# Optimization experiments

Measured on AMD Instinct MI355X. Metric: run time of the kernel, lower is better.

Reference implementation:

```python
import jax, jax.numpy as jnp
import numpy as np

N_NODES = 100000
N_EDGES = 600000
D = 128
HEADS = 8
REL = 9
N_GRAPHS = 64


def _relconv(h, coeff, basis, w_loop, b, src, dst, etypes, n_nodes):
    # DGL RelGraphConv, basis regularizer (num_bases == num_rels), sum aggregation,
    # self-loop, bias, relu activation (dropout inactive at eval).
    W = jnp.einsum('rb,bio->rio', coeff, basis)  # [REL, D, D]
    hsrc = h[src]                                # [E, D] gather
    msg = jnp.zeros((hsrc.shape[0], W.shape[2]), h.dtype)
    for r in range(REL):  # small fixed relation set
        msg = msg + jnp.where((etypes == r)[:, None], hsrc @ W[r], 0.0)
    agg = jax.ops.segment_sum(msg, dst, num_segments=n_nodes)
    return jax.nn.relu(agg + h @ w_loop + b)


def _graph_norm(x, seg, n_graphs, w, b, ms):
    # scatter-based per-subgraph normalization (graphNorm)
    counts = jax.ops.segment_sum(jnp.ones((x.shape[0],), x.dtype), seg, num_segments=n_graphs)[:, None]
    mean = jax.ops.segment_sum(x, seg, num_segments=n_graphs) / counts
    sub = x - mean[seg] * ms
    var = jax.ops.segment_sum(sub * sub, seg, num_segments=n_graphs) / counts
    std = jnp.sqrt(var + 1e-6)
    return w * sub / std[seg] + b


def _layer_norm(x, g, b):
    mu = x.mean(-1, keepdims=True)
    v = jnp.mean((x - mu) ** 2, -1, keepdims=True)
    return g * (x - mu) / jnp.sqrt(v + 1e-5) + b


def _forward(h, src, dst, etypes, seg, num_graphs,
             q_coeff, q_basis, q_loop, q_bias,
             k_coeff, k_basis, k_loop, k_bias,
             v_coeff, v_basis, v_loop, v_bias,
             o_w, o_b, gn1_w, gn1_b, gn1_ms, ln1_g, ln1_b,
             gn2_w, gn2_b, gn2_ms, ffn1_w, ffn1_b, ffn2_w, ffn2_b,
             ln2_g, ln2_b):
    n = h.shape[0]
    hn = _graph_norm(h, seg, num_graphs, gn1_w, gn1_b, gn1_ms)
    Q = _relconv(hn, q_coeff, q_basis, q_loop, q_bias, src, dst, etypes, n)
    K = _relconv(hn, k_coeff, k_basis, k_loop, k_bias, src, dst, etypes, n)
    V = _relconv(hn, v_coeff, v_basis, v_loop, v_bias, src, dst, etypes, n)
    dh = D // HEADS
    Qh = Q.reshape(n, HEADS, dh)
    Kh = K.reshape(n, HEADS, dh)
    Vh = V.reshape(n, HEADS, dh)
    # edge dot-product attention: score_e = <K[src], Q[dst]> per head
    score = (Kh[src] * Qh[dst]).sum(-1, keepdims=True)            # [E, H, 1]
    score = jnp.exp(jnp.clip(score / np.float32(np.sqrt(dh)), -10.0, 10.0))
    wV = jax.ops.segment_sum(Vh[src] * score, dst, num_segments=n)  # [N, H, dh]
    z = jax.ops.segment_sum(score, dst, num_segments=n)             # [N, H, 1]
    attn = (wV / (z + 1e-6)).reshape(n, D)
    hO = attn @ o_w + o_b
    h1 = _layer_norm(hO, ln1_g, ln1_b)
    h2 = _graph_norm(h1, seg, num_graphs, gn2_w, gn2_b, gn2_ms)
    h3 = jax.nn.relu(h2 @ ffn1_w + ffn1_b) @ ffn2_w + ffn2_b
    return _layer_norm(h3, ln2_g, ln2_b)


def setup_inputs() -> dict:
    key = jax.random.key(0)
    ks = jax.random.split(key, 32)
    s = np.float32(1.0 / np.sqrt(D))
    inp = {
        'h': jax.random.normal(ks[0], (N_NODES, D), jnp.float32),
        'src': jax.random.randint(ks[1], (N_EDGES,), 0, N_NODES),
        'dst': jax.random.randint(ks[2], (N_EDGES,), 0, N_NODES),
        'etypes': jax.random.randint(ks[3], (N_EDGES,), 0, REL),
        'seg': jnp.sort(jax.random.randint(ks[4], (N_NODES,), 0, N_GRAPHS)),
        'num_graphs': N_GRAPHS,
    }
    def lin(k, i, o):
        return jax.random.normal(k, (i, o), jnp.float32) / np.float32(np.sqrt(i))
    for idx, nm in enumerate(['q', 'k', 'v']):
        base = 5 + idx * 4
        inp[nm + '_coeff'] = jax.random.normal(ks[base], (REL, REL), jnp.float32) / np.float32(np.sqrt(REL))
        inp[nm + '_basis'] = jax.random.normal(ks[base + 1], (REL, D, D), jnp.float32) * s
        inp[nm + '_loop'] = lin(ks[base + 2], D, D)
        inp[nm + '_bias'] = jnp.zeros((D,), jnp.float32)
    inp['o_w'] = lin(ks[17], D, D)
    inp['o_b'] = jnp.zeros((D,), jnp.float32)
    for nm in ['gn1', 'gn2']:
        inp[nm + '_w'] = jnp.ones((D,), jnp.float32)
        inp[nm + '_b'] = jnp.zeros((D,), jnp.float32)
        inp[nm + '_ms'] = jnp.ones((D,), jnp.float32)
    inp['ln1_g'] = jnp.ones((D,), jnp.float32)
    inp['ln1_b'] = jnp.zeros((D,), jnp.float32)
    inp['ln2_g'] = jnp.ones((D,), jnp.float32)
    inp['ln2_b'] = jnp.zeros((D,), jnp.float32)
    inp['ffn1_w'] = lin(ks[18], D, 2 * D)
    inp['ffn1_b'] = jnp.zeros((2 * D,), jnp.float32)
    inp['ffn2_w'] = lin(ks[19], 2 * D, D)
    inp['ffn2_b'] = jnp.zeros((D,), jnp.float32)
    return inp


def reference(h, src, dst, etypes, seg, num_graphs,
              q_coeff, q_basis, q_loop, q_bias,
              k_coeff, k_basis, k_loop, k_bias,
              v_coeff, v_basis, v_loop, v_bias,
              o_w, o_b, gn1_w, gn1_b, gn1_ms, ln1_g, ln1_b,
              gn2_w, gn2_b, gn2_ms, ffn1_w, ffn1_b, ffn2_w, ffn2_b,
              ln2_g, ln2_b):
    return _forward(h, src, dst, etypes, seg, num_graphs,
                    q_coeff, q_basis, q_loop, q_bias,
                    k_coeff, k_basis, k_loop, k_bias,
                    v_coeff, v_basis, v_loop, v_bias,
                    o_w, o_b, gn1_w, gn1_b, gn1_ms, ln1_g, ln1_b,
                    gn2_w, gn2_b, gn2_ms, ffn1_w, ffn1_b, ffn2_w, ffn2_b,
                    ln2_g, ln2_b)
```

## Files before the change

kernel.cpp:

```cpp
#include <hip/hip_runtime.h>
#include <math.h>

#define N_NODES 100000
#define N_EDGES 600000
#define D 128
#define REL 9
#define NG 64

typedef float f32x4 __attribute__((ext_vector_type(4)));
typedef _Float16 f16x8 __attribute__((ext_vector_type(8)));

__device__ __forceinline__ ushort f2h(float x) {
    union { _Float16 h; ushort u; } c; c.h = (_Float16)x; return c.u;
}
__device__ __forceinline__ float h2f(ushort u) {
    union { ushort u; _Float16 h; } c; c.u = u; return (float)c.h;
}

__device__ __forceinline__ void ld16(const ushort* g, ushort* l) {
    __builtin_amdgcn_global_load_lds(
        (const __attribute__((address_space(1))) unsigned int*)g,
        (__attribute__((address_space(3))) unsigned int*)l, 16, 0, 0);
}

__device__ __forceinline__ int lbound(const int* __restrict__ a, int n, int key) {
    int lo = 0, hi = n;
    while (lo < hi) { int mid = (lo + hi) >> 1; if (a[mid] < key) lo = mid + 1; else hi = mid; }
    return lo;
}

__global__ void hist_kernel(const int* __restrict__ dst, int* __restrict__ cnt) {
    int e = blockIdx.x * 256 + threadIdx.x;
    if (e < N_EDGES) atomicAdd(&cnt[dst[e]], 1);
}

__global__ void scan1_kernel(const int* __restrict__ cnt, int* __restrict__ excl,
                             int* __restrict__ bsum, int n) {
    __shared__ int s[1024];
    int tid = threadIdx.x;
    int i = blockIdx.x * 1024 + tid;
    int v = (i < n) ? cnt[i] : 0;
    s[tid] = v;
    __syncthreads();
    for (int off = 1; off < 1024; off <<= 1) {
        int t = (tid >= off) ? s[tid - off] : 0;
        __syncthreads();
        s[tid] += t;
        __syncthreads();
    }
    if (i < n) excl[i] = s[tid] - v;
    if (tid == 1023) bsum[blockIdx.x] = s[1023];
}

__global__ void scan2_kernel(int* __restrict__ bsum, int nb) {
    __shared__ int s[128];
    int tid = threadIdx.x;
    int v = (tid < nb) ? bsum[tid] : 0;
    s[tid] = v;
    __syncthreads();
    for (int off = 1; off < 128; off <<= 1) {
        int t = (tid >= off) ? s[tid - off] : 0;
        __syncthreads();
        s[tid] += t;
        __syncthreads();
    }
    if (tid < nb) bsum[tid] = s[tid] - v;
}

__global__ void scan3_kernel(int* __restrict__ excl, const int* __restrict__ bsum, int n) {
    int i = blockIdx.x * 1024 + threadIdx.x;
    if (i < n) excl[i] += bsum[blockIdx.x];
}

__global__ void scatter_kernel(const int* __restrict__ src, const int* __restrict__ dst,
                               const int* __restrict__ ety, const int* __restrict__ estart,
                               int* __restrict__ cur, int* __restrict__ ssrc,
                               int* __restrict__ setp) {
    int e = blockIdx.x * 256 + threadIdx.x;
    if (e < N_EDGES) {
        int d = dst[e];
        int pos = estart[d] + atomicAdd(&cur[d], 1);
        ssrc[pos] = src[e];
        setp[pos] = ety[e];
    }
}

__global__ __launch_bounds__(256)
void gn_stats(const float* __restrict__ x, const int* __restrict__ seg,
              float* __restrict__ gsum, float* __restrict__ gsumsq) {
    int ch = threadIdx.x & 127;
    int rr = threadIdx.x >> 7;
    int n0 = blockIdx.x * 128;
    int nend = min(n0 + 128, N_NODES);
    float sx = 0.f, sxx = 0.f;
    int cg = -1;
    for (int n = n0 + rr; n < nend; n += 2) {
        int g = seg[n];
        if (g != cg) {
            if (cg >= 0) { atomicAdd(&gsum[cg * D + ch], sx); atomicAdd(&gsumsq[cg * D + ch], sxx); }
            cg = g; sx = 0.f; sxx = 0.f;
        }
        float v = x[(size_t)n * D + ch];
        sx += v; sxx += v * v;
    }
    if (cg >= 0) { atomicAdd(&gsum[cg * D + ch], sx); atomicAdd(&gsumsq[cg * D + ch], sxx); }
}

__global__ __launch_bounds__(256)
void gn_stats_h(const ushort* __restrict__ x, const int* __restrict__ seg,
                float* __restrict__ gsum, float* __restrict__ gsumsq) {
    int ch = threadIdx.x & 127;
    int rr = threadIdx.x >> 7;
    int n0 = blockIdx.x * 128;
    int nend = min(n0 + 128, N_NODES);
    float sx = 0.f, sxx = 0.f;
    int cg = -1;
    for (int n = n0 + rr; n < nend; n += 2) {
        int g = seg[n];
        if (g != cg) {
            if (cg >= 0) { atomicAdd(&gsum[cg * D + ch], sx); atomicAdd(&gsumsq[cg * D + ch], sxx); }
            cg = g; sx = 0.f; sxx = 0.f;
        }
        float v = h2f(x[(size_t)n * D + ch]);
        sx += v; sxx += v * v;
    }
    if (cg >= 0) { atomicAdd(&gsum[cg * D + ch], sx); atomicAdd(&gsumsq[cg * D + ch], sxx); }
}

__global__ void gn_final(const float* __restrict__ gsum, const float* __restrict__ gsumsq,
                         const int* __restrict__ seg, const float* __restrict__ w,
                         const float* __restrict__ b, const float* __restrict__ ms,
                         float* __restrict__ sc, float* __restrict__ off) {
    int g = blockIdx.x, ch = threadIdx.x;
    int lo = lbound(seg, N_NODES, g), hi = lbound(seg, N_NODES, g + 1);
    float cnt = (float)max(hi - lo, 1);
    float mean = gsum[g * D + ch] / cnt;
    float mm = mean * ms[ch];
    float var = gsumsq[g * D + ch] / cnt - 2.f * mm * mean + mm * mm;
    float rstd = rsqrtf(var + 1e-6f);
    float s = w[ch] * rstd;
    sc[g * D + ch] = s;
    off[g * D + ch] = b[ch] - s * mm;
}

__global__ __launch_bounds__(256)
void gn_apply(const float* __restrict__ x, const int* __restrict__ seg,
              const float* __restrict__ sc, const float* __restrict__ off,
              ushort* __restrict__ outhf) {
    int t = blockIdx.x * 256 + threadIdx.x;
    int n = t >> 6;
    if (n >= N_NODES) return;
    int ch = (t & 63) * 2;
    int g = seg[n];
    float2 xv = *(const float2*)&x[(size_t)n * D + ch];
    float2 s2 = *(const float2*)&sc[g * D + ch];
    float2 o2 = *(const float2*)&off[g * D + ch];
    ushort2 o;
    o.x = f2h(s2.x * xv.x + o2.x);
    o.y = f2h(s2.y * xv.y + o2.y);
    *(ushort2*)&outhf[(size_t)n * D + ch] = o;
}

__global__ __launch_bounds__(256)
void gn_apply_h(const ushort* __restrict__ x, const int* __restrict__ seg,
                const float* __restrict__ sc, const float* __restrict__ off,
                ushort* __restrict__ outhf) {
    int t = blockIdx.x * 256 + threadIdx.x;
    int n = t >> 6;
    if (n >= N_NODES) return;
    int ch = (t & 63) * 2;
    int g = seg[n];
    ushort2 xv = *(const ushort2*)&x[(size_t)n * D + ch];
    float2 s2 = *(const float2*)&sc[g * D + ch];
    float2 o2 = *(const float2*)&off[g * D + ch];
    ushort2 o;
    o.x = f2h(s2.x * h2f(xv.x) + o2.x);
    o.y = f2h(s2.y * h2f(xv.y) + o2.y);
    *(ushort2*)&outhf[(size_t)n * D + ch] = o;
}

__global__ void build_bt_qkv(const float* __restrict__ coeff, const float* __restrict__ basis,
                             const float* __restrict__ loop_w, const float* __restrict__ bias_in,
                             ushort* __restrict__ Bt, float* __restrict__ bias_out) {
    int t = blockIdx.x * 256 + threadIdx.x;
    if (t < 128) bias_out[t] = bias_in[t];
    if (t >= 128 * 1280) return;
    int o = t / 1280;
    int k = t - o * 1280;
    float v;
    if (k < 128) {
        v = loop_w[k * 128 + o];
    } else {
        int kk = k - 128;
        int r = kk >> 7, i = kk & 127;
        v = 0.f;
#pragma unroll
        for (int b = 0; b < REL; ++b)
            v += coeff[r * REL + b] * basis[((size_t)b * 128 + i) * 128 + o];
    }
    Bt[(size_t)o * 1280 + k] = f2h(v);
}

__global__ void transpose_cast(const float* __restrict__ W, int I, int O, ushort* __restrict__ Bt) {
    int t = blockIdx.x * 256 + threadIdx.x;
    if (t >= I * O) return;
    int n = t / I, k = t - n * I;
    Bt[(size_t)n * I + k] = f2h(W[(size_t)k * O + n]);
}

__global__ __launch_bounds__(256)
void s_pass(const ushort* __restrict__ hnhf, const int* __restrict__ ssrc,
            const int* __restrict__ setp, const int* __restrict__ estart,
            const int* __restrict__ ecnt, ushort* __restrict__ Ab, int c0, int c1) {
    int n = c0 + ((blockIdx.x * 256 + threadIdx.x) >> 6);
    if (n >= c1) return;
    int lane = threadIdx.x & 63;
    int e0 = estart[n], e1 = e0 + ecnt[n];
    float ax0=0,ay0=0,ax1=0,ay1=0,ax2=0,ay2=0,ax3=0,ay3=0,ax4=0,ay4=0;
    float ax5=0,ay5=0,ax6=0,ay6=0,ax7=0,ay7=0,ax8=0,ay8=0;
    for (int e = e0; e < e1; ++e) {
        int s = ssrc[e];
        int r = __builtin_amdgcn_readfirstlane(setp[e]);
        ushort2 hv = *(const ushort2*)&hnhf[(size_t)s * D + 2 * lane];
        float vx = h2f(hv.x), vy = h2f(hv.y);
        switch (r) {
            case 0: ax0 += vx; ay0 += vy; break;
            case 1: ax1 += vx; ay1 += vy; break;
            case 2: ax2 += vx; ay2 += vy; break;
            case 3: ax3 += vx; ay3 += vy; break;
            case 4: ax4 += vx; ay4 += vy; break;
            case 5: ax5 += vx; ay5 += vy; break;
            case 6: ax6 += vx; ay6 += vy; break;
            case 7: ax7 += vx; ay7 += vy; break;
            default: ax8 += vx; ay8 += vy; break;
        }
    }
    ushort* arow = Ab + (size_t)(n - c0) * 1152;
    ushort2 t;
#define ST(r) t.x = f2h(ax##r); t.y = f2h(ay##r); *(ushort2*)&arow[r * 128 + 2 * lane] = t;
    ST(0) ST(1) ST(2) ST(3) ST(4) ST(5) ST(6) ST(7) ST(8)
#undef ST
}

template<bool SPLITA, bool RELU, bool F16OUT>
__global__ __launch_bounds__(256, 3)
void mfma_gemm(const ushort* __restrict__ A1, const ushort* __restrict__ A2, int lda2, int M,
               const ushort* __restrict__ Bt, int K,
               const float* __restrict__ bias, void* __restrict__ Cout, int ldc) {
    __shared__ ushort As[128 * 64];
    __shared__ ushort Bs[128 * 64];
    const int tid = threadIdx.x;
    const int lane = tid & 63;
    const int wave = tid >> 6;
    const int wm = wave & 1, wn = wave >> 1;
    const int quad = lane >> 4, l16 = lane & 15;
    const int col0 = blockIdx.x * 128, row0 = blockIdx.y * 128;

    const ushort* sA1[4];
    const ushort* sA2[4];
    const ushort* sB[4];
#pragma unroll
    for (int i = 0; i < 4; ++i) {
        int rs = (wave * 4 + i) * 8 + (lane >> 3);
        int kg = (lane & 7) ^ (rs & 7);
        int ra = row0 + rs; if (ra >= M) ra = M - 1;
        sA1[i] = SPLITA ? (A1 + (size_t)ra * 128 + kg * 8) : nullptr;
        sA2[i] = A2 + (size_t)ra * lda2 + kg * 8;
        sB[i]  = Bt + (size_t)(col0 + rs) * K + kg * 8;
    }

    f32x4 acc[4][4];
#pragma unroll
    for (int i = 0; i < 4; ++i)
#pragma unroll
        for (int j = 0; j < 4; ++j) acc[i][j] = (f32x4){0.f, 0.f, 0.f, 0.f};

    for (int kc = 0; kc < K; kc += 64) {
#pragma unroll
        for (int i = 0; i < 4; ++i) {
            const ushort* as = (SPLITA && kc < 128) ? (sA1[i] + kc) : (sA2[i] + (SPLITA ? kc - 128 : kc));
            ld16(as, &As[(wave * 4 + i) * 512]);
            ld16(sB[i] + kc, &Bs[(wave * 4 + i) * 512]);
        }
        __syncthreads();
#pragma unroll
        for (int h = 0; h < 2; ++h) {
            f16x8 af[4], bf[4];
#pragma unroll
            for (int i = 0; i < 4; ++i) {
                int r = wm * 64 + i * 16 + l16;
                af[i] = *(const f16x8*)&As[r * 64 + (((h * 4 + quad) ^ (r & 7)) * 8)];
                int c = wn * 64 + i * 16 + l16;
                bf[i] = *(const f16x8*)&Bs[c * 64 + (((h * 4 + quad) ^ (c & 7)) * 8)];
            }
#pragma unroll
            for (int i = 0; i < 4; ++i)
#pragma unroll
                for (int j = 0; j < 4; ++j)
                    acc[i][j] = __builtin_amdgcn_mfma_f32_16x16x32_f16(af[i], bf[j], acc[i][j], 0, 0, 0);
        }
        __syncthreads();
    }

#pragma unroll
    for (int i = 0; i < 4; ++i) {
        int gr0 = row0 + wm * 64 + i * 16 + quad * 4;
#pragma unroll
        for (int r = 0; r < 4; ++r) {
            int grow = gr0 + r;
            if (grow >= M) continue;
#pragma unroll
            for (int j = 0; j < 4; ++j) {
                int gcol = col0 + wn * 64 + j * 16 + l16;
                float v = acc[i][j][r] + bias[gcol];
                if (RELU) v = fmaxf(v, 0.f);
                if (F16OUT) ((ushort*)Cout)[(size_t)grow * ldc + gcol] = f2h(v);
                else        ((float*)Cout)[(size_t)grow * ldc + gcol] = v;
            }
        }
    }
}

template<bool F16OUT>
__global__ __launch_bounds__(256, 3)
void mfma_gemm_ln(const ushort* __restrict__ A, int lda, int M,
                  const ushort* __restrict__ Bt, int K,
                  const float* __restrict__ bias, const float* __restrict__ lng,
                  const float* __restrict__ lnb, void* __restrict__ Cout) {
    __shared__ ushort As[128 * 64];
    __shared__ ushort Bs[128 * 64];
    __shared__ float rsum[2][128];
    __shared__ float rsq[2][128];
    const int tid = threadIdx.x;
    const int lane = tid & 63;
    const int wave = tid >> 6;
    const int wm = wave & 1, wn = wave >> 1;
    const int quad = lane >> 4, l16 = lane & 15;
    const int row0 = blockIdx.y * 128;

    const ushort* sA[4];
    const ushort* sB[4];
#pragma unroll
    for (int i = 0; i < 4; ++i) {
        int rs = (wave * 4 + i) * 8 + (lane >> 3);
        int kg = (lane & 7) ^ (rs & 7);
        int ra = row0 + rs; if (ra >= M) ra = M - 1;
        sA[i] = A + (size_t)ra * lda + kg * 8;
        sB[i] = Bt + (size_t)rs * K + kg * 8;
    }

    f32x4 acc[4][4];
#pragma unroll
    for (int i = 0; i < 4; ++i)
#pragma unroll
        for (int j = 0; j < 4; ++j) acc[i][j] = (f32x4){0.f, 0.f, 0.f, 0.f};

    for (int kc = 0; kc < K; kc += 64) {
#pragma unroll
        for (int i = 0; i < 4; ++i) {
            ld16(sA[i] + kc, &As[(wave * 4 + i) * 512]);
            ld16(sB[i] + kc, &Bs[(wave * 4 + i) * 512]);
        }
        __syncthreads();
#pragma unroll
        for (int h = 0; h < 2; ++h) {
            f16x8 af[4], bf[4];
#pragma unroll
            for (int i = 0; i < 4; ++i) {
                int r = wm * 64 + i * 16 + l16;
                af[i] = *(const f16x8*)&As[r * 64 + (((h * 4 + quad) ^ (r & 7)) * 8)];
                int c = wn * 64 + i * 16 + l16;
                bf[i] = *(const f16x8*)&Bs[c * 64 + (((h * 4 + quad) ^ (c & 7)) * 8)];
            }
#pragma unroll
            for (int i = 0; i < 4; ++i)
#pragma unroll
                for (int j = 0; j < 4; ++j)
                    acc[i][j] = __builtin_amdgcn_mfma_f32_16x16x32_f16(af[i], bf[j], acc[i][j], 0, 0, 0);
        }
        __syncthreads();
    }

#pragma unroll
    for (int i = 0; i < 4; ++i) {
#pragma unroll
        for (int r = 0; r < 4; ++r) {
            float s = 0.f, q = 0.f;
#pragma unroll
            for (int j = 0; j < 4; ++j) {
                float v = acc[i][j][r] + bias[wn * 64 + j * 16 + l16];
                s += v; q += v * v;
            }
            s += __shfl_xor(s, 1); q += __shfl_xor(q, 1);
            s += __shfl_xor(s, 2); q += __shfl_xor(q, 2);
            s += __shfl_xor(s, 4); q += __shfl_xor(q, 4);
            s += __shfl_xor(s, 8); q += __shfl_xor(q, 8);
            if (l16 == 0) {
                int row = wm * 64 + i * 16 + quad * 4 + r;
                rsum[wn][row] = s;
                rsq[wn][row] = q;
            }
        }
    }
    __syncthreads();

#pragma unroll
    for (int i = 0; i < 4; ++i) {
#pragma unroll
        for (int r = 0; r < 4; ++r) {
            int row = wm * 64 + i * 16 + quad * 4 + r;
            int grow = row0 + row;
            if (grow >= M) continue;
            float tot = rsum[0][row] + rsum[1][row];
            float tq  = rsq[0][row] + rsq[1][row];
            float mu = tot * (1.f / 128.f);
            float var = tq * (1.f / 128.f) - mu * mu;
            float rstd = rsqrtf(var + 1e-5f);
#pragma unroll
            for (int j = 0; j < 4; ++j) {
                int gcol = wn * 64 + j * 16 + l16;
                float v = acc[i][j][r] + bias[gcol];
                float o = lng[gcol] * (v - mu) * rstd + lnb[gcol];
                if (F16OUT) ((ushort*)Cout)[(size_t)grow * 128 + gcol] = f2h(o);
                else        ((float*)Cout)[(size_t)grow * 128 + gcol] = o;
            }
        }
    }
}

__global__ __launch_bounds__(256)
void attn_kernel(const ushort* __restrict__ C, const int* __restrict__ ssrc,
                 const int* __restrict__ estart, const int* __restrict__ ecnt,
                 ushort* __restrict__ attnhf) {
    int n = (blockIdx.x * 256 + threadIdx.x) >> 6;
    if (n >= N_NODES) return;
    int lane = threadIdx.x & 63;
    ushort4 qh = *(const ushort4*)&C[(size_t)n * 384 + 4 * (lane & 31)];
    float q0 = h2f(qh.x), q1 = h2f(qh.y), q2 = h2f(qh.z), q3 = h2f(qh.w);
    int e0 = estart[n], e1 = e0 + ecnt[n];
    float w0 = 0.f, w1 = 0.f, w2 = 0.f, w3 = 0.f, z = 0.f;
    const bool isK = lane < 32;
    int e = e0;
    for (; e + 2 <= e1; e += 2) {
        int s0 = ssrc[e], s1 = ssrc[e + 1];
        ushort4 a = *(const ushort4*)&C[(size_t)s0 * 384 + 128 + 4 * lane];
        ushort4 b = *(const ushort4*)&C[(size_t)s1 * 384 + 128 + 4 * lane];
        float d0 = h2f(a.x) * q0 + h2f(a.y) * q1 + h2f(a.z) * q2 + h2f(a.w) * q3;
        float d1 = h2f(b.x) * q0 + h2f(b.y) * q1 + h2f(b.z) * q2 + h2f(b.w) * q3;
        d0 += __shfl_xor(d0, 1); d1 += __shfl_xor(d1, 1);
        d0 += __shfl_xor(d0, 2); d1 += __shfl_xor(d1, 2);
        float p0 = __shfl_xor(d0, 32), p1 = __shfl_xor(d1, 32);
        d0 = isK ? d0 : p0; d1 = isK ? d1 : p1;
        float sc0 = __expf(fminf(fmaxf(d0 * 0.25f, -10.f), 10.f));
        float sc1 = __expf(fminf(fmaxf(d1 * 0.25f, -10.f), 10.f));
        w0 += sc0 * h2f(a.x) + sc1 * h2f(b.x);
        w1 += sc0 * h2f(a.y) + sc1 * h2f(b.y);
        w2 += sc0 * h2f(a.z) + sc1 * h2f(b.z);
        w3 += sc0 * h2f(a.w) + sc1 * h2f(b.w);
        z += sc0 + sc1;
    }
    if (e < e1) {
        int s0 = ssrc[e];
        ushort4 a = *(const ushort4*)&C[(size_t)s0 * 384 + 128 + 4 * lane];
        float d0 = h2f(a.x) * q0 + h2f(a.y) * q1 + h2f(a.z) * q2 + h2f(a.w) * q3;
        d0 += __shfl_xor(d0, 1);
        d0 += __shfl_xor(d0, 2);
        float p0 = __shfl_xor(d0, 32);
        d0 = isK ? d0 : p0;
        float sc0 = __expf(fminf(fmaxf(d0 * 0.25f, -10.f), 10.f));
        w0 += sc0 * h2f(a.x); w1 += sc0 * h2f(a.y);
        w2 += sc0 * h2f(a.z); w3 += sc0 * h2f(a.w);
        z += sc0;
    }
    if (!isK) {
        float inv = 1.f / (z + 1e-6f);
        ushort4 o;
        o.x = f2h(w0 * inv); o.y = f2h(w1 * inv);
        o.z = f2h(w2 * inv); o.w = f2h(w3 * inv);
        *(ushort4*)&attnhf[(size_t)n * D + 4 * (lane - 32)] = o;
    }
}

extern "C" void kernel_launch(void* const* d_in, const int* in_sizes, int n_in,
                              void* d_out, int out_size, void* d_ws, size_t ws_size,
                              hipStream_t stream) {
    (void)in_sizes; (void)n_in; (void)out_size;
    const float* h     = (const float*)d_in[0];
    const int*   src   = (const int*)d_in[1];
    const int*   dst   = (const int*)d_in[2];
    const int*   ety   = (const int*)d_in[3];
    const int*   seg   = (const int*)d_in[4];
    const float* coeffs[3] = {(const float*)d_in[6],  (const float*)d_in[10], (const float*)d_in[14]};
    const float* bases [3] = {(const float*)d_in[7],  (const float*)d_in[11], (const float*)d_in[15]};
    const float* loops [3] = {(const float*)d_in[8],  (const float*)d_in[12], (const float*)d_in[16]};
    const float* pbias [3] = {(const float*)d_in[9],  (const float*)d_in[13], (const float*)d_in[17]};
    const float* o_w   = (const float*)d_in[18];
    const float* o_b   = (const float*)d_in[19];
    const float* gn1_w = (const float*)d_in[20];
    const float* gn1_b = (const float*)d_in[21];
    const float* gn1_ms= (const float*)d_in[22];
    const float* gn2_w = (const float*)d_in[23];
    const float* gn2_b = (const float*)d_in[24];
    const float* gn2_ms= (const float*)d_in[25];
    const float* ln1_g = (const float*)d_in[26];
    const float* ln1_b = (const float*)d_in[27];
    const float* ln2_g = (const float*)d_in[28];
    const float* ln2_b = (const float*)d_in[29];
    const float* ffn1_w= (const float*)d_in[30];
    const float* ffn1_b= (const float*)d_in[31];
    const float* ffn2_w= (const float*)d_in[32];
    const float* ffn2_b= (const float*)d_in[33];

    char* p = (char*)d_ws;
    auto take = [&](size_t bytes) { char* r = p; p += (bytes + 255) & ~(size_t)255; return r; };
    int*    ecnt   = (int*)take((size_t)N_NODES * 4);
    int*    estart = (int*)take((size_t)N_NODES * 4);
    int*    ecur   = (int*)take((size_t)N_NODES * 4);
    int*    bsum   = (int*)take(512);
    int*    ssrc   = (int*)take((size_t)N_EDGES * 4);
    int*    setp   = (int*)take((size_t)N_EDGES * 4);
    float*  gsum   = (float*)take((size_t)NG * D * 4 * 2);
    float*  gsumsq = gsum + NG * D;
    float*  gsc    = (float*)take((size_t)NG * D * 4);
    float*  goff   = (float*)take((size_t)NG * D * 4);
    ushort* Btqkv  = (ushort*)take((size_t)384 * 1280 * 2);
    float*  biasq  = (float*)take(384 * 4);
    ushort* Bto    = (ushort*)take((size_t)128 * 128 * 2);
    ushort* Btf1   = (ushort*)take((size_t)256 * 128 * 2);
    ushort* Btf2   = (ushort*)take((size_t)128 * 256 * 2);
    ushort* hnhf   = (ushort*)take((size_t)N_NODES * D * 2);
    ushort* attnhf = (ushort*)take((size_t)N_NODES * D * 2);
    ushort* h1hf   = (ushort*)take((size_t)N_NODES * D * 2);
    ushort* Cqkv   = (ushort*)take((size_t)N_NODES * 384 * 2);
    size_t used = (size_t)(p - (char*)d_ws);
    size_t avail = (ws_size > used) ? ws_size - used : 0;
    int NC = 1;
    if (avail < (size_t)N_NODES * 1152 * 2) NC = 4;
    if (NC == 4 && avail < ((size_t)(N_NODES / 4 + 1) * 1152 * 2)) NC = 8;
    ushort* Ab = (ushort*)p;
    const int chunk = (N_NODES + NC - 1) / NC;

    ushort* gn2hf  = Cqkv;
    ushort* ffn1hf = (ushort*)((char*)Cqkv + 25600000);

    const int EB = (N_EDGES + 255) / 256;
    const int SB = (N_NODES + 1023) / 1024;
    const int WB = (N_NODES * 64 + 255) / 256;
    const int GB = (N_NODES + 127) / 128;
    const int RB = (N_NODES + 127) / 128;

    hipMemsetAsync(ecnt, 0, N_NODES * sizeof(int), stream);
    hipMemsetAsync(ecur, 0, N_NODES * sizeof(int), stream);
    hist_kernel<<<EB, 256, 0, stream>>>(dst, ecnt);
    scan1_kernel<<<SB, 1024, 0, stream>>>(ecnt, estart, bsum, N_NODES);
    scan2_kernel<<<1, 128, 0, stream>>>(bsum, SB);
    scan3_kernel<<<SB, 1024, 0, stream>>>(estart, bsum, N_NODES);
    scatter_kernel<<<EB, 256, 0, stream>>>(src, dst, ety, estart, ecur, ssrc, setp);

    for (int pj = 0; pj < 3; ++pj)
        build_bt_qkv<<<640, 256, 0, stream>>>(coeffs[pj], bases[pj], loops[pj], pbias[pj],
                                              Btqkv + (size_t)pj * 128 * 1280, biasq + pj * 128);
    transpose_cast<<<64, 256, 0, stream>>>(o_w, 128, 128, Bto);
    transpose_cast<<<128, 256, 0, stream>>>(ffn1_w, 128, 256, Btf1);
    transpose_cast<<<128, 256, 0, stream>>>(ffn2_w, 256, 128, Btf2);

    hipMemsetAsync(gsum, 0, (size_t)NG * D * 8, stream);
    gn_stats<<<GB, 256, 0, stream>>>(h, seg, gsum, gsumsq);
    gn_final<<<NG, 128, 0, stream>>>(gsum, gsumsq, seg, gn1_w, gn1_b, gn1_ms, gsc, goff);
    gn_apply<<<WB, 256, 0, stream>>>(h, seg, gsc, goff, hnhf);

    for (int c = 0; c < NC; ++c) {
        int c0 = c * chunk;
        int c1 = min(N_NODES, c0 + chunk);
        int rows = c1 - c0;
        if (rows <= 0) break;
        s_pass<<<(rows + 3) / 4, 256, 0, stream>>>(hnhf, ssrc, setp, estart, ecnt, Ab, c0, c1);
        mfma_gemm<true, true, true><<<dim3(3, (rows + 127) / 128), 256, 0, stream>>>(
            hnhf + (size_t)c0 * 128, Ab, 1152, rows, Btqkv, 1280, biasq,
            Cqkv + (size_t)c0 * 384, 384);
    }

    attn_kernel<<<WB, 256, 0, stream>>>(Cqkv, ssrc, estart, ecnt, attnhf);

    mfma_gemm_ln<true><<<dim3(1, RB), 256, 0, stream>>>(
        attnhf, 128, N_NODES, Bto, 128, o_b, ln1_g, ln1_b, h1hf);

    hipMemsetAsync(gsum, 0, (size_t)NG * D * 8, stream);
    gn_stats_h<<<GB, 256, 0, stream>>>(h1hf, seg, gsum, gsumsq);
    gn_final<<<NG, 128, 0, stream>>>(gsum, gsumsq, seg, gn2_w, gn2_b, gn2_ms, gsc, goff);
    gn_apply_h<<<WB, 256, 0, stream>>>(h1hf, seg, gsc, goff, gn2hf);

    mfma_gemm<false, true, true><<<dim3(2, RB), 256, 0, stream>>>(
        nullptr, gn2hf, 128, N_NODES, Btf1, 128, ffn1_b, ffn1hf, 256);
    mfma_gemm_ln<false><<<dim3(1, RB), 256, 0, stream>>>(
        ffn1hf, 256, N_NODES, Btf2, 256, ffn2_b, ln2_g, ln2_b, (float*)d_out);
}
```

Before: 803.3 us.

## Merge weight-prep launches, accumulate s_pass in fp16, use fdot2 attention

Weight-preparation work that used several launches now runs as one batched build kernel and one combined transpose-cast kernel. The two memsets become one by placing ecur next to ecnt. s_pass now accumulates neighbour features in packed fp16 and takes two edges per iteration. The attention kernel has every lane load both K and V and compute the score with fdot2 over an 8-lane reduction, where before half the wave loaded K, half loaded V, and scores were swapped across the wave. Launch overhead and per-edge work drop, but summing many edges in fp16 can overflow or lose precision.

```diff
diff --git a/kernel.cpp b/kernel.cpp
--- a/kernel.cpp
+++ b/kernel.cpp
@@ -9,6 +9,7 @@
 
 typedef float f32x4 __attribute__((ext_vector_type(4)));
 typedef _Float16 f16x8 __attribute__((ext_vector_type(8)));
+typedef _Float16 h16x2 __attribute__((ext_vector_type(2)));
 
 __device__ __forceinline__ ushort f2h(float x) {
     union { _Float16 h; ushort u; } c; c.h = (_Float16)x; return c.u;
@@ -179,11 +180,21 @@
     *(ushort2*)&outhf[(size_t)n * D + ch] = o;
 }
 
-__global__ void build_bt_qkv(const float* __restrict__ coeff, const float* __restrict__ basis,
-                             const float* __restrict__ loop_w, const float* __restrict__ bias_in,
-                             ushort* __restrict__ Bt, float* __restrict__ bias_out) {
+__global__ void build_bt_qkv3(const float* __restrict__ c0, const float* __restrict__ c1,
+                              const float* __restrict__ c2, const float* __restrict__ b0,
+                              const float* __restrict__ b1, const float* __restrict__ b2,
+                              const float* __restrict__ l0, const float* __restrict__ l1,
+                              const float* __restrict__ l2, const float* __restrict__ i0,
+                              const float* __restrict__ i1, const float* __restrict__ i2,
+                              ushort* __restrict__ Btqkv, float* __restrict__ biasq) {
+    int pj = blockIdx.y;
+    const float* coeff  = pj == 0 ? c0 : (pj == 1 ? c1 : c2);
+    const float* basis  = pj == 0 ? b0 : (pj == 1 ? b1 : b2);
+    const float* loop_w = pj == 0 ? l0 : (pj == 1 ? l1 : l2);
+    const float* bin    = pj == 0 ? i0 : (pj == 1 ? i1 : i2);
+    ushort* Bt = Btqkv + (size_t)pj * 128 * 1280;
     int t = blockIdx.x * 256 + threadIdx.x;
-    if (t < 128) bias_out[t] = bias_in[t];
+    if (t < 128) biasq[pj * 128 + t] = bin[t];
     if (t >= 128 * 1280) return;
     int o = t / 1280;
     int k = t - o * 1280;
@@ -201,11 +212,22 @@
     Bt[(size_t)o * 1280 + k] = f2h(v);
 }
 
-__global__ void transpose_cast(const float* __restrict__ W, int I, int O, ushort* __restrict__ Bt) {
+__global__ void transpose_cast3(const float* __restrict__ o_w, ushort* __restrict__ Bto,
+                                const float* __restrict__ f1, ushort* __restrict__ Btf1,
+                                const float* __restrict__ f2, ushort* __restrict__ Btf2) {
     int t = blockIdx.x * 256 + threadIdx.x;
-    if (t >= I * O) return;
-    int n = t / I, k = t - n * I;
-    Bt[(size_t)n * I + k] = f2h(W[(size_t)k * O + n]);
+    if (t < 16384) {
+        int n = t >> 7, k = t & 127;
+        Bto[(size_t)n * 128 + k] = f2h(o_w[(size_t)k * 128 + n]);
+    } else if (t < 49152) {
+        int u = t - 16384;
+        int n = u >> 7, k = u & 127;
+        Btf1[(size_t)n * 128 + k] = f2h(f1[(size_t)k * 256 + n]);
+    } else if (t < 81920) {
+        int u = t - 49152;
+        int n = u >> 8, k = u & 255;
+        Btf2[(size_t)n * 256 + k] = f2h(f2[(size_t)k * 128 + n]);
+    }
 }
 
 __global__ __launch_bounds__(256)
@@ -216,28 +238,31 @@
     if (n >= c1) return;
     int lane = threadIdx.x & 63;
     int e0 = estart[n], e1 = e0 + ecnt[n];
-    float ax0=0,ay0=0,ax1=0,ay1=0,ax2=0,ay2=0,ax3=0,ay3=0,ax4=0,ay4=0;
-    float ax5=0,ay5=0,ax6=0,ay6=0,ax7=0,ay7=0,ax8=0,ay8=0;
-    for (int e = e0; e < e1; ++e) {
-        int s = ssrc[e];
-        int r = __builtin_amdgcn_readfirstlane(setp[e]);
-        ushort2 hv = *(const ushort2*)&hnhf[(size_t)s * D + 2 * lane];
-        float vx = h2f(hv.x), vy = h2f(hv.y);
-        switch (r) {
-            case 0: ax0 += vx; ay0 += vy; break;
-            case 1: ax1 += vx; ay1 += vy; break;
-            case 2: ax2 += vx; ay2 += vy; break;
-            case 3: ax3 += vx; ay3 += vy; break;
-            case 4: ax4 += vx; ay4 += vy; break;
-            case 5: ax5 += vx; ay5 += vy; break;
-            case 6: ax6 += vx; ay6 += vy; break;
-            case 7: ax7 += vx; ay7 += vy; break;
-            default: ax8 += vx; ay8 += vy; break;
-        }
-    }
+    h16x2 a0 = (h16x2)0, a1 = (h16x2)0, a2 = (h16x2)0, a3 = (h16x2)0, a4 = (h16x2)0;
+    h16x2 a5 = (h16x2)0, a6 = (h16x2)0, a7 = (h16x2)0, a8 = (h16x2)0;
+#define ACC(rr, hv) switch (rr) { \
+        case 0: a0 += hv; break; case 1: a1 += hv; break; case 2: a2 += hv; break; \
+        case 3: a3 += hv; break; case 4: a4 += hv; break; case 5: a5 += hv; break; \
+        case 6: a6 += hv; break; case 7: a7 += hv; break; default: a8 += hv; break; }
+    int e = e0;
+    for (; e + 2 <= e1; e += 2) {
+        int s0 = ssrc[e], s1 = ssrc[e + 1];
+        int r0 = __builtin_amdgcn_readfirstlane(setp[e]);
+        int r1 = __builtin_amdgcn_readfirstlane(setp[e + 1]);
+        h16x2 hv0 = *(const h16x2*)&hnhf[(size_t)s0 * D + 2 * lane];
+        h16x2 hv1 = *(const h16x2*)&hnhf[(size_t)s1 * D + 2 * lane];
+        ACC(r0, hv0)
+        ACC(r1, hv1)
+    }
+    if (e < e1) {
+        int s0 = ssrc[e];
+        int r0 = __builtin_amdgcn_readfirstlane(setp[e]);
+        h16x2 hv0 = *(const h16x2*)&hnhf[(size_t)s0 * D + 2 * lane];
+        ACC(r0, hv0)
+    }
+#undef ACC
     ushort* arow = Ab + (size_t)(n - c0) * 1152;
-    ushort2 t;
-#define ST(r) t.x = f2h(ax##r); t.y = f2h(ay##r); *(ushort2*)&arow[r * 128 + 2 * lane] = t;
+#define ST(r) *(h16x2*)&arow[r * 128 + 2 * lane] = a##r;
     ST(0) ST(1) ST(2) ST(3) ST(4) ST(5) ST(6) ST(7) ST(8)
 #undef ST
 }
@@ -435,50 +460,45 @@
     int n = (blockIdx.x * 256 + threadIdx.x) >> 6;
     if (n >= N_NODES) return;
     int lane = threadIdx.x & 63;
-    ushort4 qh = *(const ushort4*)&C[(size_t)n * 384 + 4 * (lane & 31)];
-    float q0 = h2f(qh.x), q1 = h2f(qh.y), q2 = h2f(qh.z), q3 = h2f(qh.w);
+    h16x2 qh = *(const h16x2*)&C[(size_t)n * 384 + 2 * lane];
     int e0 = estart[n], e1 = e0 + ecnt[n];
-    float w0 = 0.f, w1 = 0.f, w2 = 0.f, w3 = 0.f, z = 0.f;
-    const bool isK = lane < 32;
+    float wvx = 0.f, wvy = 0.f, z = 0.f;
     int e = e0;
     for (; e + 2 <= e1; e += 2) {
         int s0 = ssrc[e], s1 = ssrc[e + 1];
-        ushort4 a = *(const ushort4*)&C[(size_t)s0 * 384 + 128 + 4 * lane];
-        ushort4 b = *(const ushort4*)&C[(size_t)s1 * 384 + 128 + 4 * lane];
-        float d0 = h2f(a.x) * q0 + h2f(a.y) * q1 + h2f(a.z) * q2 + h2f(a.w) * q3;
-        float d1 = h2f(b.x) * q0 + h2f(b.y) * q1 + h2f(b.z) * q2 + h2f(b.w) * q3;
+        h16x2 k0 = *(const h16x2*)&C[(size_t)s0 * 384 + 128 + 2 * lane];
+        h16x2 k1 = *(const h16x2*)&C[(size_t)s1 * 384 + 128 + 2 * lane];
+        h16x2 v0 = *(const h16x2*)&C[(size_t)s0 * 384 + 256 + 2 * lane];
+        h16x2 v1 = *(const h16x2*)&C[(size_t)s1 * 384 + 256 + 2 * lane];
+        float d0 = __builtin_amdgcn_fdot2(k0, qh, 0.f, false);
+        float d1 = __builtin_amdgcn_fdot2(k1, qh, 0.f, false);
         d0 += __shfl_xor(d0, 1); d1 += __shfl_xor(d1, 1);
         d0 += __shfl_xor(d0, 2); d1 += __shfl_xor(d1, 2);
-        float p0 = __shfl_xor(d0, 32), p1 = __shfl_xor(d1, 32);
-        d0 = isK ? d0 : p0; d1 = isK ? d1 : p1;
+        d0 += __shfl_xor(d0, 4); d1 += __shfl_xor(d1, 4);
         float sc0 = __expf(fminf(fmaxf(d0 * 0.25f, -10.f), 10.f));
         float sc1 = __expf(fminf(fmaxf(d1 * 0.25f, -10.f), 10.f));
-        w0 += sc0 * h2f(a.x) + sc1 * h2f(b.x);
-        w1 += sc0 * h2f(a.y) + sc1 * h2f(b.y);
-        w2 += sc0 * h2f(a.z) + sc1 * h2f(b.z);
-        w3 += sc0 * h2f(a.w) + sc1 * h2f(b.w);
+        wvx += sc0 * (float)v0.x + sc1 * (float)v1.x;
+        wvy += sc0 * (float)v0.y + sc1 * (float)v1.y;
         z += sc0 + sc1;
     }
     if (e < e1) {
         int s0 = ssrc[e];
-        ushort4 a = *(const ushort4*)&C[(size_t)s0 * 384 + 128 + 4 * lane];
-        float d0 = h2f(a.x) * q0 + h2f(a.y) * q1 + h2f(a.z) * q2 + h2f(a.w) * q3;
+        h16x2 k0 = *(const h16x2*)&C[(size_t)s0 * 384 + 128 + 2 * lane];
+        h16x2 v0 = *(const h16x2*)&C[(size_t)s0 * 384 + 256 + 2 * lane];
+        float d0 = __builtin_amdgcn_fdot2(k0, qh, 0.f, false);
         d0 += __shfl_xor(d0, 1);
         d0 += __shfl_xor(d0, 2);
-        float p0 = __shfl_xor(d0, 32);
-        d0 = isK ? d0 : p0;
+        d0 += __shfl_xor(d0, 4);
         float sc0 = __expf(fminf(fmaxf(d0 * 0.25f, -10.f), 10.f));
-        w0 += sc0 * h2f(a.x); w1 += sc0 * h2f(a.y);
-        w2 += sc0 * h2f(a.z); w3 += sc0 * h2f(a.w);
+        wvx += sc0 * (float)v0.x;
+        wvy += sc0 * (float)v0.y;
         z += sc0;
     }
-    if (!isK) {
-        float inv = 1.f / (z + 1e-6f);
-        ushort4 o;
-        o.x = f2h(w0 * inv); o.y = f2h(w1 * inv);
-        o.z = f2h(w2 * inv); o.w = f2h(w3 * inv);
-        *(ushort4*)&attnhf[(size_t)n * D + 4 * (lane - 32)] = o;
-    }
+    float inv = 1.f / (z + 1e-6f);
+    ushort2 o;
+    o.x = f2h(wvx * inv);
+    o.y = f2h(wvy * inv);
+    *(ushort2*)&attnhf[(size_t)n * D + 2 * lane] = o;
 }
 
 extern "C" void kernel_launch(void* const* d_in, const int* in_sizes, int n_in,
@@ -514,8 +534,8 @@
     char* p = (char*)d_ws;
     auto take = [&](size_t bytes) { char* r = p; p += (bytes + 255) & ~(size_t)255; return r; };
     int*    ecnt   = (int*)take((size_t)N_NODES * 4);
+    int*    ecur   = (int*)take((size_t)N_NODES * 4);
     int*    estart = (int*)take((size_t)N_NODES * 4);
-    int*    ecur   = (int*)take((size_t)N_NODES * 4);
     int*    bsum   = (int*)take(512);
     int*    ssrc   = (int*)take((size_t)N_EDGES * 4);
     int*    setp   = (int*)take((size_t)N_EDGES * 4);
@@ -549,20 +569,17 @@
     const int GB = (N_NODES + 127) / 128;
     const int RB = (N_NODES + 127) / 128;
 
-    hipMemsetAsync(ecnt, 0, N_NODES * sizeof(int), stream);
-    hipMemsetAsync(ecur, 0, N_NODES * sizeof(int), stream);
+    hipMemsetAsync(ecnt, 0, (size_t)((char*)(estart) - (char*)ecnt), stream);
     hist_kernel<<<EB, 256, 0, stream>>>(dst, ecnt);
     scan1_kernel<<<SB, 1024, 0, stream>>>(ecnt, estart, bsum, N_NODES);
     scan2_kernel<<<1, 128, 0, stream>>>(bsum, SB);
     scan3_kernel<<<SB, 1024, 0, stream>>>(estart, bsum, N_NODES);
     scatter_kernel<<<EB, 256, 0, stream>>>(src, dst, ety, estart, ecur, ssrc, setp);
 
-    for (int pj = 0; pj < 3; ++pj)
-        build_bt_qkv<<<640, 256, 0, stream>>>(coeffs[pj], bases[pj], loops[pj], pbias[pj],
-                                              Btqkv + (size_t)pj * 128 * 1280, biasq + pj * 128);
-    transpose_cast<<<64, 256, 0, stream>>>(o_w, 128, 128, Bto);
-    transpose_cast<<<128, 256, 0, stream>>>(ffn1_w, 128, 256, Btf1);
-    transpose_cast<<<128, 256, 0, stream>>>(ffn2_w, 256, 128, Btf2);
+    build_bt_qkv3<<<dim3(640, 3), 256, 0, stream>>>(
+        coeffs[0], coeffs[1], coeffs[2], bases[0], bases[1], bases[2],
+        loops[0], loops[1], loops[2], pbias[0], pbias[1], pbias[2], Btqkv, biasq);
+    transpose_cast3<<<320, 256, 0, stream>>>(o_w, Bto, ffn1_w, Btf1, ffn2_w, Btf2);
 
     hipMemsetAsync(gsum, 0, (size_t)NG * D * 8, stream);
     gn_stats<<<GB, 256, 0, stream>>>(h, seg, gsum, gsumsq);
```

After: 767.5 us. -4.5%, faster.
